# Kernel tuning notes

Measured on AMD Instinct MI355X. Metric: run time of the kernel, lower is better.

The kernel has to match this reference:

```python
import jax, jax.numpy as jnp
import numpy as np

FEATURE_DIM = 256
NUM_HASHES = 128
NUM_NODES = 500000
NUM_SEGMENTS = 512


def setup_inputs() -> dict:
    key = jax.random.key(0)
    k_x, k_b, k_h = jax.random.split(key, 3)
    x = jax.random.normal(k_x, (NUM_NODES, FEATURE_DIM), dtype=jnp.float32)
    batch = jnp.sort(jax.random.randint(k_b, (NUM_NODES,), 0, NUM_SEGMENTS, dtype=jnp.int64))
    hash_matrices = jax.random.normal(k_h, (NUM_HASHES, FEATURE_DIM), dtype=jnp.float32)
    return {"x": x, "batch": batch, "num_segments": NUM_SEGMENTS, "hash_matrices": hash_matrices}


def reference(x, batch, num_segments, hash_matrices):
    # hash_values: [num_nodes, num_hashes]
    hash_values = jnp.matmul(x, hash_matrices.T)
    # per-graph (segment) min over nodes -> [num_segments, num_hashes]
    sketch = jax.ops.segment_min(hash_values, batch, num_segments=num_segments)
    # torch leaves empty groups at zero; empty segments come back +inf here
    sketch = jnp.where(jnp.isinf(sketch), jnp.zeros_like(sketch), sketch)
    return sketch
```

## Files before the change

### kernel.cpp

```cpp
#include <hip/hip_runtime.h>


#define M_NODES 500000
#define KDIM    256
#define NHASH   128
#define NSEG    512

#define BM 128
#define BK 32
#define XSTR (BK + 1)

__device__ __forceinline__ unsigned int enc_f(float f) {
    unsigned int b = __float_as_uint(f);
    return (b & 0x80000000u) ? ~b : (b | 0x80000000u);
}

__global__ void ht_transpose(const float* __restrict__ H, float* __restrict__ Ht) {
    const int t = blockIdx.x * 256 + threadIdx.x;
    const int k = t >> 7;
    const int h = t & 127;
    Ht[t] = H[h * KDIM + k];
}

__global__ __launch_bounds__(256, 4)
void minhash_main(const float* __restrict__ x,
                  const unsigned int* __restrict__ batch_raw,
                  const float* __restrict__ Ht,
                  unsigned int* __restrict__ ws) {
    __shared__ float2 xsp[(BM / 2) * XSTR];
    float* lds = (float*)xsp;

    const int tid  = threadIdx.x;
    const int lane = tid & 63;
    const int w32 = __builtin_amdgcn_readfirstlane(tid >> 6) * 32;
    const int blockBase = blockIdx.x * BM;

    float acc0[32], acc1[32];
    #pragma unroll
    for (int j = 0; j < 32; ++j) { acc0[j] = 0.0f; acc1[j] = 0.0f; }

    for (int k0 = 0; k0 < KDIM; k0 += BK) {
        #pragma unroll
        for (int i = 0; i < 4; ++i) {
            const int idx = tid + 256 * i;
            const int n   = idx >> 3;
            const int f4  = idx & 7;
            const int gn  = blockBase + n;
            float4 v = make_float4(0.f, 0.f, 0.f, 0.f);
            if (gn < M_NODES)
                v = *(const float4*)(x + (size_t)gn * KDIM + k0 + f4 * 4);
            const int base = (n >> 1) * (2 * XSTR) + (n & 1) + f4 * 8;
            lds[base + 0] = v.x;
            lds[base + 2] = v.y;
            lds[base + 4] = v.z;
            lds[base + 6] = v.w;
        }
        __syncthreads();

        const float* hko = Ht + (size_t)k0 * NHASH + w32;
        #pragma unroll 4
        for (int kk = 0; kk < BK; ++kk) {
            const float2 xv = xsp[lane * XSTR + kk];
            const float* hk = hko + kk * NHASH;
            #pragma unroll
            for (int j = 0; j < 32; ++j) {
                const float hv = hk[j];
                acc0[j] = fmaf(xv.x, hv, acc0[j]);
                acc1[j] = fmaf(xv.y, hv, acc1[j]);
            }
        }
        __syncthreads();
    }

    const bool is64 = (batch_raw[499999] == 0u);
    const long long* b64 = (const long long*)batch_raw;
    const int*       b32 = (const int*)batch_raw;

    const int gn0 = blockBase + 2 * lane;
    const int gn1 = gn0 + 1;
    int seg0 = -1, seg1 = -1;
    if (gn0 < M_NODES) seg0 = is64 ? (int)b64[gn0] : b32[gn0];
    if (gn1 < M_NODES) seg1 = is64 ? (int)b64[gn1] : b32[gn1];

    float v[32];
    int seg;
    if (seg0 == seg1) {
        seg = seg0;
        #pragma unroll
        for (int j = 0; j < 32; ++j) v[j] = fminf(acc0[j], acc1[j]);
    } else {
        if (seg0 >= 0) {
            #pragma unroll
            for (int j = 0; j < 32; ++j)
                atomicMin(&ws[seg0 * NHASH + w32 + j], enc_f(acc0[j]));
        }
        seg = seg1;
        #pragma unroll
        for (int j = 0; j < 32; ++j) v[j] = acc1[j];
    }

    #pragma unroll
    for (int d = 1; d < 64; d <<= 1) {
        const int  oseg = __shfl_down(seg, d, 64);
        const bool ok   = (lane + d < 64) && (oseg == seg);
        #pragma unroll
        for (int j = 0; j < 32; ++j) {
            const float ov = __shfl_down(v[j], d, 64);
            if (ok) v[j] = fminf(v[j], ov);
        }
    }

    const int pseg = __shfl_up(seg, 1, 64);
    if (seg >= 0 && (lane == 0 || pseg != seg)) {
        #pragma unroll
        for (int j = 0; j < 32; ++j)
            atomicMin(&ws[seg * NHASH + w32 + j], enc_f(v[j]));
    }
}

__global__ void minhash_finalize(const unsigned int* __restrict__ ws,
                                 float* __restrict__ out) {
    const int i = blockIdx.x * blockDim.x + threadIdx.x;
    if (i < NSEG * NHASH) {
        const unsigned int u = ws[i];
        out[i] = (u == 0xFFFFFFFFu)
                     ? 0.0f
                     : ((u & 0x80000000u) ? __uint_as_float(u ^ 0x80000000u)
                                          : __uint_as_float(~u));
    }
}

extern "C" void kernel_launch(void* const* d_in, const int* in_sizes, int n_in,
                              void* d_out, int out_size, void* d_ws, size_t ws_size,
                              hipStream_t stream) {
    const float* x = (const float*)d_in[0];
    const unsigned int* batch = (const unsigned int*)d_in[1];
    const float* H = (const float*)d_in[3];

    unsigned int* ws_atomic = (unsigned int*)d_ws;
    float* Ht = (float*)d_ws + NSEG * NHASH;

    hipMemsetAsync(d_ws, 0xFF, NSEG * NHASH * sizeof(unsigned int), stream);
    ht_transpose<<<(KDIM * NHASH) / 256, 256, 0, stream>>>(H, Ht);

    const int grid = (M_NODES + BM - 1) / BM;
    minhash_main<<<grid, 256, 0, stream>>>(x, batch, Ht, ws_atomic);
    minhash_finalize<<<(NSEG * NHASH + 255) / 256, 256, 0, stream>>>(ws_atomic, (float*)d_out);
}
```

Baseline: 856.9 us.

## Replace FP32 FMA GEMM with split-bf16 MFMA emulation and LDS-staged segment min

The scalar FP32 FMA inner product is replaced by bf16 MFMA 16x16x32 instructions. Both x and the hash matrix are split into high and low bf16 parts, and four MFMAs per tile give near-FP32 accuracy. The hash matrix is pre-split into an MFMA-friendly fragment layout, and the accumulators are staged through LDS in two halves for the existing shuffle-based segment min and atomics. It trades a 4x MFMA count, on-the-fly bf16 conversion and extra LDS traffic for the far higher matrix-core throughput, with a small risk of precision differences against the FP32 reference.

```diff
diff --git a/kernel.cpp b/kernel.cpp
--- a/kernel.cpp
+++ b/kernel.cpp
@@ -6,115 +6,191 @@
 #define NHASH   128
 #define NSEG    512
 
-#define BM 128
-#define BK 32
-#define XSTR (BK + 1)
-
+#define BM     128
+#define BK     32
+#define NCHUNK (KDIM / BK)
+
+typedef __attribute__((ext_vector_type(8))) short bf16x8;
+typedef __attribute__((ext_vector_type(4))) float f32x4;
+
+__device__ __forceinline__ unsigned short f2bf(float f) {
+    unsigned int u = __float_as_uint(f);
+    u += 0x7FFFu + ((u >> 16) & 1u);
+    return (unsigned short)(u >> 16);
+}
+__device__ __forceinline__ float bf2f(unsigned short s) {
+    return __uint_as_float(((unsigned int)s) << 16);
+}
 __device__ __forceinline__ unsigned int enc_f(float f) {
     unsigned int b = __float_as_uint(f);
     return (b & 0x80000000u) ? ~b : (b | 0x80000000u);
 }
 
-__global__ void ht_transpose(const float* __restrict__ H, float* __restrict__ Ht) {
+__global__ void hsplit(const float* __restrict__ H,
+                       unsigned short* __restrict__ b1f,
+                       unsigned short* __restrict__ b2f) {
     const int t = blockIdx.x * 256 + threadIdx.x;
-    const int k = t >> 7;
-    const int h = t & 127;
-    Ht[t] = H[h * KDIM + k];
-}
-
-__global__ __launch_bounds__(256, 4)
+    const int n = t >> 8;
+    const int k = t & 255;
+    const float h = H[t];
+    const unsigned short s1 = f2bf(h);
+    const unsigned short s2 = f2bf(h - bf2f(s1));
+    const int idx = ((k >> 5) * 8 + (n >> 4)) * 512 + (((k >> 3) & 3) * 16 + (n & 15)) * 8 + (k & 7);
+    b1f[idx] = s1;
+    b2f[idx] = s2;
+}
+
+#define ATILE 576
+#define AKG   144
+
+__global__ __launch_bounds__(256, 3)
 void minhash_main(const float* __restrict__ x,
                   const unsigned int* __restrict__ batch_raw,
-                  const float* __restrict__ Ht,
+                  const unsigned short* __restrict__ b1f,
+                  const unsigned short* __restrict__ b2f,
                   unsigned int* __restrict__ ws) {
-    __shared__ float2 xsp[(BM / 2) * XSTR];
-    float* lds = (float*)xsp;
+    __shared__ __align__(16) char smem[34816];
+    unsigned short* a1 = (unsigned short*)smem;
+    unsigned short* a2 = a1 + 4608;
+    unsigned short* b1 = a1 + 9216;
+    unsigned short* b2 = a1 + 13312;
+    float* sc = (float*)smem;
 
     const int tid  = threadIdx.x;
     const int lane = tid & 63;
-    const int w32 = __builtin_amdgcn_readfirstlane(tid >> 6) * 32;
-    const int blockBase = blockIdx.x * BM;
-
-    float acc0[32], acc1[32];
+    const int w    = __builtin_amdgcn_readfirstlane(tid >> 6);
+    const int quad = lane >> 4;
+    const int c16  = lane & 15;
+    const int rh   = w & 1;
+    const int ch   = w >> 1;
+    const long long blockBase = (long long)blockIdx.x * BM;
+
+    f32x4 acc[4][4];
     #pragma unroll
-    for (int j = 0; j < 32; ++j) { acc0[j] = 0.0f; acc1[j] = 0.0f; }
-
-    for (int k0 = 0; k0 < KDIM; k0 += BK) {
-        #pragma unroll
-        for (int i = 0; i < 4; ++i) {
-            const int idx = tid + 256 * i;
-            const int n   = idx >> 3;
-            const int f4  = idx & 7;
-            const int gn  = blockBase + n;
-            float4 v = make_float4(0.f, 0.f, 0.f, 0.f);
-            if (gn < M_NODES)
-                v = *(const float4*)(x + (size_t)gn * KDIM + k0 + f4 * 4);
-            const int base = (n >> 1) * (2 * XSTR) + (n & 1) + f4 * 8;
-            lds[base + 0] = v.x;
-            lds[base + 2] = v.y;
-            lds[base + 4] = v.z;
-            lds[base + 6] = v.w;
-        }
-        __syncthreads();
-
-        const float* hko = Ht + (size_t)k0 * NHASH + w32;
-        #pragma unroll 4
-        for (int kk = 0; kk < BK; ++kk) {
-            const float2 xv = xsp[lane * XSTR + kk];
-            const float* hk = hko + kk * NHASH;
-            #pragma unroll
-            for (int j = 0; j < 32; ++j) {
-                const float hv = hk[j];
-                acc0[j] = fmaf(xv.x, hv, acc0[j]);
-                acc1[j] = fmaf(xv.y, hv, acc1[j]);
+    for (int rt = 0; rt < 4; ++rt)
+        #pragma unroll
+        for (int ct = 0; ct < 4; ++ct)
+            acc[rt][ct] = (f32x4){0.f, 0.f, 0.f, 0.f};
+
+    for (int chunk = 0; chunk < NCHUNK; ++chunk) {
+        const int k0 = chunk * BK;
+
+        {
+            const float4* gb1 = (const float4*)(b1f + chunk * 4096);
+            const float4* gb2 = (const float4*)(b2f + chunk * 4096);
+            ((float4*)b1)[tid]       = gb1[tid];
+            ((float4*)b1)[tid + 256] = gb1[tid + 256];
+            ((float4*)b2)[tid]       = gb2[tid];
+            ((float4*)b2)[tid + 256] = gb2[tid + 256];
+        }
+        #pragma unroll
+        for (int pass = 0; pass < 4; ++pass) {
+            const int r  = (tid >> 3) + pass * 32;
+            const int f4 = tid & 7;
+            const long long gr = blockBase + r;
+            float4 vv = make_float4(0.f, 0.f, 0.f, 0.f);
+            if (gr < (long long)M_NODES)
+                vv = *(const float4*)(x + gr * KDIM + k0 + f4 * 4);
+            const unsigned short h1x = f2bf(vv.x), h1y = f2bf(vv.y),
+                                 h1z = f2bf(vv.z), h1w = f2bf(vv.w);
+            const unsigned short l1x = f2bf(vv.x - bf2f(h1x)), l1y = f2bf(vv.y - bf2f(h1y)),
+                                 l1z = f2bf(vv.z - bf2f(h1z)), l1w = f2bf(vv.w - bf2f(h1w));
+            const int base = (r >> 4) * ATILE + (f4 >> 1) * AKG + (r & 15) * 8 + (f4 & 1) * 4;
+            uint2 p1, p2;
+            p1.x = (unsigned)h1x | ((unsigned)h1y << 16);
+            p1.y = (unsigned)h1z | ((unsigned)h1w << 16);
+            p2.x = (unsigned)l1x | ((unsigned)l1y << 16);
+            p2.y = (unsigned)l1z | ((unsigned)l1w << 16);
+            *(uint2*)(a1 + base) = p1;
+            *(uint2*)(a2 + base) = p2;
+        }
+        __syncthreads();
+
+        bf16x8 a1f[4], a2f[4];
+        #pragma unroll
+        for (int rt = 0; rt < 4; ++rt) {
+            const int off = (rh * 4 + rt) * ATILE + quad * AKG + c16 * 8;
+            a1f[rt] = *(const bf16x8*)(a1 + off);
+            a2f[rt] = *(const bf16x8*)(a2 + off);
+        }
+        #pragma unroll
+        for (int ct = 0; ct < 4; ++ct) {
+            const int boff = ((ch * 4 + ct) * 64 + lane) * 8;
+            const bf16x8 b1v = *(const bf16x8*)(b1 + boff);
+            const bf16x8 b2v = *(const bf16x8*)(b2 + boff);
+            #pragma unroll
+            for (int rt = 0; rt < 4; ++rt) {
+                acc[rt][ct] = __builtin_amdgcn_mfma_f32_16x16x32_bf16(a1f[rt], b1v, acc[rt][ct], 0, 0, 0);
+                acc[rt][ct] = __builtin_amdgcn_mfma_f32_16x16x32_bf16(a2f[rt], b1v, acc[rt][ct], 0, 0, 0);
+                acc[rt][ct] = __builtin_amdgcn_mfma_f32_16x16x32_bf16(a1f[rt], b2v, acc[rt][ct], 0, 0, 0);
+                acc[rt][ct] = __builtin_amdgcn_mfma_f32_16x16x32_bf16(a2f[rt], b2v, acc[rt][ct], 0, 0, 0);
             }
         }
         __syncthreads();
     }
 
     const bool is64 = (batch_raw[499999] == 0u);
-    const long long* b64 = (const long long*)batch_raw;
-    const int*       b32 = (const int*)batch_raw;
-
-    const int gn0 = blockBase + 2 * lane;
-    const int gn1 = gn0 + 1;
+    const long long* bb64 = (const long long*)batch_raw;
+    const int*       bb32 = (const int*)batch_raw;
+
+    const int p = lane;
+    const int cg = w;
+    const long long gn0 = blockBase + 2 * p;
+    const long long gn1 = gn0 + 1;
     int seg0 = -1, seg1 = -1;
-    if (gn0 < M_NODES) seg0 = is64 ? (int)b64[gn0] : b32[gn0];
-    if (gn1 < M_NODES) seg1 = is64 ? (int)b64[gn1] : b32[gn1];
-
-    float v[32];
-    int seg;
-    if (seg0 == seg1) {
-        seg = seg0;
-        #pragma unroll
-        for (int j = 0; j < 32; ++j) v[j] = fminf(acc0[j], acc1[j]);
-    } else {
-        if (seg0 >= 0) {
-            #pragma unroll
-            for (int j = 0; j < 32; ++j)
-                atomicMin(&ws[seg0 * NHASH + w32 + j], enc_f(acc0[j]));
-        }
-        seg = seg1;
-        #pragma unroll
-        for (int j = 0; j < 32; ++j) v[j] = acc1[j];
-    }
-
-    #pragma unroll
-    for (int d = 1; d < 64; d <<= 1) {
-        const int  oseg = __shfl_down(seg, d, 64);
-        const bool ok   = (lane + d < 64) && (oseg == seg);
-        #pragma unroll
-        for (int j = 0; j < 32; ++j) {
-            const float ov = __shfl_down(v[j], d, 64);
-            if (ok) v[j] = fminf(v[j], ov);
-        }
-    }
-
-    const int pseg = __shfl_up(seg, 1, 64);
-    if (seg >= 0 && (lane == 0 || pseg != seg)) {
-        #pragma unroll
-        for (int j = 0; j < 32; ++j)
-            atomicMin(&ws[seg * NHASH + w32 + j], enc_f(v[j]));
+    if (gn0 < (long long)M_NODES) seg0 = is64 ? (int)bb64[gn0] : bb32[gn0];
+    if (gn1 < (long long)M_NODES) seg1 = is64 ? (int)bb64[gn1] : bb32[gn1];
+
+    for (int h = 0; h < 2; ++h) {
+        if (ch == h) {
+            #pragma unroll
+            for (int ct = 0; ct < 4; ++ct) {
+                #pragma unroll
+                for (int rt = 0; rt < 4; ++rt) {
+                    const int node = rh * 64 + rt * 16 + quad * 4;
+                    const int colp = ct * 16 + c16;
+                    *(f32x4*)(sc + colp * 132 + node) = acc[rt][ct];
+                }
+            }
+        }
+        __syncthreads();
+
+        float v[16];
+        int seg;
+        if (seg0 == seg1) {
+            seg = seg0;
+            #pragma unroll
+            for (int j = 0; j < 16; ++j) {
+                const float2 nv = *(const float2*)(sc + (cg * 16 + j) * 132 + 2 * p);
+                v[j] = fminf(nv.x, nv.y);
+            }
+        } else {
+            seg = seg1;
+            #pragma unroll
+            for (int j = 0; j < 16; ++j) {
+                const float2 nv = *(const float2*)(sc + (cg * 16 + j) * 132 + 2 * p);
+                if (seg0 >= 0)
+                    atomicMin(&ws[seg0 * NHASH + h * 64 + cg * 16 + j], enc_f(nv.x));
+                v[j] = nv.y;
+            }
+        }
+        #pragma unroll
+        for (int d = 1; d < 64; d <<= 1) {
+            const int  oseg = __shfl_down(seg, d, 64);
+            const bool ok   = (lane + d < 64) && (oseg == seg);
+            #pragma unroll
+            for (int j = 0; j < 16; ++j) {
+                const float ov = __shfl_down(v[j], d, 64);
+                if (ok) v[j] = fminf(v[j], ov);
+            }
+        }
+        const int pseg = __shfl_up(seg, 1, 64);
+        if (seg >= 0 && (lane == 0 || pseg != seg)) {
+            #pragma unroll
+            for (int j = 0; j < 16; ++j)
+                atomicMin(&ws[seg * NHASH + h * 64 + cg * 16 + j], enc_f(v[j]));
+        }
+        __syncthreads();
     }
 }
 
@@ -137,13 +213,14 @@
     const unsigned int* batch = (const unsigned int*)d_in[1];
     const float* H = (const float*)d_in[3];
 
-    unsigned int* ws_atomic = (unsigned int*)d_ws;
-    float* Ht = (float*)d_ws + NSEG * NHASH;
+    unsigned int*   ws  = (unsigned int*)d_ws;
+    unsigned short* b1f = (unsigned short*)((char*)d_ws + 256 * 1024);
+    unsigned short* b2f = (unsigned short*)((char*)d_ws + 320 * 1024);
 
     hipMemsetAsync(d_ws, 0xFF, NSEG * NHASH * sizeof(unsigned int), stream);
-    ht_transpose<<<(KDIM * NHASH) / 256, 256, 0, stream>>>(H, Ht);
+    hsplit<<<(KDIM * NHASH) / 256, 256, 0, stream>>>(H, b1f, b2f);
 
     const int grid = (M_NODES + BM - 1) / BM;
-    minhash_main<<<grid, 256, 0, stream>>>(x, batch, Ht, ws_atomic);
-    minhash_finalize<<<(NSEG * NHASH + 255) / 256, 256, 0, stream>>>(ws_atomic, (float*)d_out);
-}
+    minhash_main<<<grid, 256, 0, stream>>>(x, batch, b1f, b2f, ws);
+    minhash_finalize<<<(NSEG * NHASH + 255) / 256, 256, 0, stream>>>(ws, (float*)d_out);
+}
```

Measured after the change: 731.6 us. 1.17x faster.
